# Optimization experiments

Hardware: AMD Instinct MI355X
Metric: run time of the kernel (lower is better)

The kernel has to match this reference:

```python
import jax, jax.numpy as jnp
import numpy as np

NEG_SLOPE = 0.2
K_L = 0.5
K_G = 0.5
TEMP_G = 1e-3


def _leaky(v):
    return jnp.where(v >= 0, v, NEG_SLOPE * v)


def _topk_row_mask(scores, keep):
    # scores: [n, n, h]; torch.topk(dim=0) -> indices [keep, n] per head,
    # then head_mask[indices, :] = 1 selects whole ROWS (any column hit).
    n = scores.shape[0]
    s = jnp.transpose(scores, (1, 2, 0))        # [n_cols, h, n_rows]
    _, idx = jax.lax.top_k(s, keep)             # [n_cols, h, keep]

    def per_head(idx_h):                        # idx_h: [n_cols, keep]
        return jnp.zeros((n,), scores.dtype).at[idx_h.reshape(-1)].set(1.0)

    rows = jax.vmap(per_head, in_axes=1, out_axes=0)(idx)  # [h, n_rows]
    return jnp.transpose(rows)[:, None, :]      # [n_rows, 1, h] broadcast over cols


def setup_inputs() -> dict:
    key = jax.random.key(0)
    ks = jax.random.split(key, 8)
    n, in_f, feat_dim = 1024, 256, 128
    H, F = 4, 64                                # n_heads, n_hidden (out_features=256)
    feats = jax.random.normal(ks[0], (n, feat_dim), dtype=jnp.float32)
    x = jax.random.normal(ks[1], (n, in_f), dtype=jnp.float32)
    adj = jax.random.randint(ks[2], (n, n, 1), 0, 2).astype(jnp.int32)
    sc = 0.05
    W_l = jax.random.normal(ks[3], (in_f, H * F), dtype=jnp.float32) * sc
    W_r = jax.random.normal(ks[4], (in_f, H * F), dtype=jnp.float32) * sc
    attn_w = jax.random.normal(ks[5], (F,), dtype=jnp.float32) * sc
    W_delta = jax.random.normal(ks[6], (2 * F, F), dtype=jnp.float32) * sc
    b_delta = jnp.zeros((F,), dtype=jnp.float32)
    return {"feats": feats, "x": x, "adj": adj, "W_l": W_l, "W_r": W_r,
            "attn_w": attn_w, "W_delta": W_delta, "b_delta": b_delta}


def reference(feats, x, adj, W_l, W_r, attn_w, W_delta, b_delta):
    n = x.shape[0]
    F = attn_w.shape[0]
    H = W_l.shape[1] // F
    g_l = (x @ W_l).reshape(n, H, F)
    g_r = (x @ W_r).reshape(n, H, F)
    # g_sum[i, j] = g_l[j] + g_r[i]  (repeat vs repeat_interleave ordering)
    g_sum = g_r[:, None, :, :] + g_l[None, :, :, :]          # [n, n, H, F]
    e = jnp.einsum('ijhf,f->ijh', _leaky(g_sum), attn_w)     # [n, n, H]

    mask_adj = adj > 0                                        # [n, n, 1]
    a_l = jax.nn.softmax(jnp.where(mask_adj, e, -jnp.inf), axis=1)
    a_1nd = a_l * mask_adj.astype(e.dtype)

    keep_l = int(n * (1.0 - K_L))
    a_filt = a_1nd * _topk_row_mask(a_1nd, keep_l)
    attn_local = jnp.einsum('ijh,jhf->ihf', a_filt, g_r)     # [n, H, F]

    omega = jax.nn.softmax(e, axis=1)
    fn = (feats - feats.min(axis=0)) / (feats.max(axis=0) - feats.min(axis=0))
    fn = jnp.where(jnp.isnan(fn), 0.0, fn)
    g_rn = (g_r - g_r.min(axis=0)) / (g_r.max(axis=0) - g_r.min(axis=0))
    nf = jnp.linalg.norm(fn, axis=1)                          # [n] (index j)
    ng = jnp.linalg.norm(g_rn, axis=2)                        # [n, H] (index i)
    alpha = jax.nn.softmax(jnp.abs(nf[None, :, None] - ng[:, None, :]), axis=1)
    gamma = 0.5 * (omega + (1.0 - alpha))

    keep_g = int(n * (1.0 - K_G))
    gf = gamma * _topk_row_mask(gamma, keep_g)
    gf = jax.nn.softmax(jnp.where(gf == 0, 1e-10, gf) / TEMP_G, axis=1)
    attn_global = jnp.einsum('ijh,jhf->ihf', gf, g_r)         # [n, H, F]

    inter = _leaky(jnp.concatenate([attn_local, attn_global], axis=2) @ W_delta + b_delta)
    delta = jax.nn.softmax(inter, axis=1)                     # softmax over heads (torch dim=1)
    attn_res = delta * attn_local + (1.0 - delta) * attn_global
    return attn_res.reshape(n, H * F)
```

## Files before the change

### kernel.cpp

```cpp
#include <hip/hip_runtime.h>
#include <cstdint>
#include <cstddef>

#define N 1024
#define HN 4
#define FDIM 64
#define KSEL 512
#define FLT_MAX_ 3.402823466e+38f

__device__ __forceinline__ float wred_sum(float v){
#pragma unroll
  for(int o=32;o>0;o>>=1) v += __shfl_down(v,o,64);
  return v;
}
__device__ __forceinline__ float bfly_sum(float v){
#pragma unroll
  for(int o=1;o<64;o<<=1) v += __shfl_xor(v,o,64);
  return v;
}
__device__ __forceinline__ float bfly_max(float v){
#pragma unroll
  for(int o=1;o<64;o<<=1) v = fmaxf(v,__shfl_xor(v,o,64));
  return v;
}
__device__ __forceinline__ int bfly_sumi(int v){
#pragma unroll
  for(int o=1;o<64;o<<=1) v += __shfl_xor(v,o,64);
  return v;
}
__device__ __forceinline__ float bred_sum(float v, float* scr){
  int t=threadIdx.x;
  v = wred_sum(v);
  __syncthreads();
  if((t&63)==0) scr[t>>6]=v;
  __syncthreads();
  return (scr[0]+scr[1])+(scr[2]+scr[3]);
}

__global__ __launch_bounds__(256) void stage1(const float* __restrict__ x,
                                              const float* __restrict__ W_l,
                                              const float* __restrict__ W_r,
                                              const int* __restrict__ adj,
                                              const float* __restrict__ feats,
                                              float* __restrict__ g_l,
                                              float* __restrict__ g_r,
                                              unsigned* __restrict__ adjbit,
                                              int* __restrict__ masks,
                                              float* __restrict__ pmin_f,
                                              float* __restrict__ pmax_f){
  int bx = blockIdx.x, t = threadIdx.x;
  if(bx < 512){
    const float* __restrict__ W = (bx >= 256) ? W_r : W_l;
    float* __restrict__ g = (bx >= 256) ? g_r : g_l;
    int i0 = (bx & 255)*4;
    float acc[4] = {0.f,0.f,0.f,0.f};
#pragma unroll 8
    for(int k=0;k<256;k++){
      float w = W[(size_t)k*256 + t];
#pragma unroll
      for(int r=0;r<4;r++) acc[r] = fmaf(x[(size_t)(i0+r)*256 + k], w, acc[r]);
    }
#pragma unroll
    for(int r=0;r<4;r++) g[(size_t)(i0+r)*256 + t] = acc[r];
  } else if(bx < 1536){
    int i = bx - 512, w = t>>6, lane = t&63;
    if(i < 32) masks[i*256 + t] = 0;
#pragma unroll
    for(int it=0; it<4; it++){
      int j = w*256 + it*64 + lane;
      int v = adj[(size_t)i*N + j];
      unsigned long long mb = __ballot(v > 0);
      if(lane == 0){
        adjbit[i*32 + w*8 + it*2]     = (unsigned)mb;
        adjbit[i*32 + w*8 + it*2 + 1] = (unsigned)(mb >> 32);
      }
    }
  } else {
    int chunk = bx - 1536;
    if(t < 128){
      float lo = FLT_MAX_, hi = -FLT_MAX_;
      int r0 = chunk*64;
      for(int r=0;r<64;r++){
        float v = feats[(size_t)(r0+r)*128 + t];
        lo = fminf(lo,v); hi = fmaxf(hi,v);
      }
      pmin_f[chunk*128+t]=lo; pmax_f[chunk*128+t]=hi;
    }
  }
}

__global__ __launch_bounds__(256) void stage2(const float* __restrict__ g_l,
                                              const float* __restrict__ g_r,
                                              const float* __restrict__ attn_w,
                                              const float* __restrict__ feats,
                                              const float* __restrict__ pmin_f, const float* __restrict__ pmax_f,
                                              float* __restrict__ pmin_g, float* __restrict__ pmax_g,
                                              float* __restrict__ nf,
                                              float* __restrict__ e,
                                              float* __restrict__ eT){
  __shared__ __align__(16) float smem[2*64*68 + 128];
  int bx = blockIdx.x, t = threadIdx.x;
  if(bx < 1024){
    float* grs = smem;
    float* gls = smem + 64*68;
    float* aw  = smem + 2*64*68;
    float* aw2 = aw + 64;
    int h = bx >> 8, i0 = ((bx>>4)&15)*64, j0 = (bx&15)*64;
    if(t < 64){ float w = attn_w[t]; aw[t]=w; aw2[t]=0.2f*w; }
#pragma unroll
    for(int k=0;k<16;k++){
      int idx = t + k*256; int r = idx>>6, f = idx&63;
      grs[r*68+f] = g_r[(size_t)(i0+r)*256 + h*64 + f];
      gls[r*68+f] = g_l[(size_t)(j0+r)*256 + h*64 + f];
    }
    __syncthreads();
    int tj = t&15, ti = t>>4;
    float acc[4][4];
#pragma unroll
    for(int a=0;a<4;a++)
#pragma unroll
      for(int b=0;b<4;b++) acc[a][b]=0.f;
    for(int fc=0; fc<64; fc+=4){
      float4 wv  = *(float4*)&aw[fc];
      float4 wv2 = *(float4*)&aw2[fc];
      float4 ga4[4], gb4[4];
#pragma unroll
      for(int a=0;a<4;a++) ga4[a] = *(float4*)&grs[(ti*4+a)*68+fc];
#pragma unroll
      for(int b=0;b<4;b++) gb4[b] = *(float4*)&gls[(tj+16*b)*68+fc];
#pragma unroll
      for(int a=0;a<4;a++)
#pragma unroll
        for(int b=0;b<4;b++){
          float s0 = ga4[a].x + gb4[b].x;
          float s1 = ga4[a].y + gb4[b].y;
          float s2 = ga4[a].z + gb4[b].z;
          float s3 = ga4[a].w + gb4[b].w;
          acc[a][b] = fmaf(s0, (s0>=0.f)?wv.x:wv2.x, acc[a][b]);
          acc[a][b] = fmaf(s1, (s1>=0.f)?wv.y:wv2.y, acc[a][b]);
          acc[a][b] = fmaf(s2, (s2>=0.f)?wv.z:wv2.z, acc[a][b]);
          acc[a][b] = fmaf(s3, (s3>=0.f)?wv.w:wv2.w, acc[a][b]);
        }
    }
#pragma unroll
    for(int a=0;a<4;a++)
#pragma unroll
      for(int b=0;b<4;b++){
        int i = i0 + ti*4 + a, j = j0 + tj + 16*b;
        e[((size_t)h*N + i)*N + j] = acc[a][b];
      }
    __syncthreads();
    float* esT = smem;
#pragma unroll
    for(int a=0;a<4;a++)
#pragma unroll
      for(int b=0;b<4;b++)
        esT[(tj + 16*b)*68 + ti*4 + a] = acc[a][b];
    __syncthreads();
#pragma unroll
    for(int k=0;k<4;k++){
      int jl = (t>>4) + 16*k, ilx = (t&15)*4;
      *(float4*)(eT + ((size_t)h*N + j0 + jl)*N + i0 + ilx) = *(float4*)&esT[jl*68 + ilx];
    }
  } else if(bx < 1040){
    int chunk = bx - 1024;
    float lo = FLT_MAX_, hi = -FLT_MAX_;
    int r0 = chunk*64;
    for(int r=0;r<64;r++){
      float v = g_r[(size_t)(r0+r)*256 + t];
      lo = fminf(lo,v); hi = fmaxf(hi,v);
    }
    pmin_g[chunk*256+t]=lo; pmax_g[chunk*256+t]=hi;
  } else {
    int i = bx - 1040;
    float* scr = smem;
    float u = 0.f;
    if(t < 128){
      float lo = FLT_MAX_, hi = -FLT_MAX_;
#pragma unroll
      for(int k=0;k<16;k++){
        lo = fminf(lo, pmin_f[k*128+t]);
        hi = fmaxf(hi, pmax_f[k*128+t]);
      }
      float d = hi - lo;
      float v = feats[(size_t)i*128 + t];
      u = (d==0.f) ? 0.f : (v - lo)/d;
    }
    float tot = bred_sum(u*u, scr);
    if(t==0) nf[i] = sqrtf(tot);
  }
}

__global__ __launch_bounds__(256) void row_stats(const float* __restrict__ e,
                                                 const unsigned* __restrict__ adjbit,
                                                 const float* __restrict__ nf,
                                                 const float* __restrict__ g_r,
                                                 const float* __restrict__ pmin_g, const float* __restrict__ pmax_g,
                                                 float* __restrict__ ng,
                                                 float* __restrict__ mlA, float* __restrict__ islA,
                                                 float* __restrict__ moA, float* __restrict__ isoA,
                                                 float* __restrict__ maA, float* __restrict__ isaA,
                                                 float* __restrict__ mgA, float* __restrict__ sgA){
  int i = blockIdx.x, t = threadIdx.x, h = t>>6, lane = t&63;
  float glo = FLT_MAX_, ghi = -FLT_MAX_;
#pragma unroll
  for(int k=0;k<16;k++){
    glo = fminf(glo, pmin_g[k*256 + h*64 + lane]);
    ghi = fmaxf(ghi, pmax_g[k*256 + h*64 + lane]);
  }
  float dg = ghi - glo;
  float ug = (g_r[(size_t)i*256 + h*64 + lane] - glo)/dg;
  float ngv = sqrtf(bfly_sum(ug*ug));
  if(lane==0) ng[h*N + i] = ngv;

  size_t base = ((size_t)h*N + i)*N;
  float er[16], nfr[16];
  unsigned nib[4];
#pragma unroll
  for(int c=0;c<4;c++){
    float4 e4 = *(const float4*)(e  + base + c*256 + lane*4);
    float4 n4 = *(const float4*)(nf + c*256 + lane*4);
    er[c*4+0]=e4.x; er[c*4+1]=e4.y; er[c*4+2]=e4.z; er[c*4+3]=e4.w;
    nfr[c*4+0]=n4.x; nfr[c*4+1]=n4.y; nfr[c*4+2]=n4.z; nfr[c*4+3]=n4.w;
    nib[c] = (adjbit[i*32 + c*8 + (lane>>3)] >> ((lane&7)*4)) & 0xFu;
  }
  float ml=-FLT_MAX_, mo=-FLT_MAX_, ma=-FLT_MAX_;
#pragma unroll
  for(int c=0;c<4;c++)
#pragma unroll
    for(int k=0;k<4;k++){
      int q = c*4+k;
      float ev = er[q];
      mo = fmaxf(mo, ev);
      if((nib[c]>>k)&1) ml = fmaxf(ml, ev);
      ma = fmaxf(ma, fabsf(nfr[q]-ngv));
    }
  ml = bfly_max(ml); mo = bfly_max(mo); ma = bfly_max(ma);
  float sl=0.f, so=0.f, sa=0.f;
#pragma unroll
  for(int c=0;c<4;c++)
#pragma unroll
    for(int k=0;k<4;k++){
      int q = c*4+k;
      float ev = er[q];
      so += __expf(ev-mo);
      if((nib[c]>>k)&1) sl += __expf(ev-ml);
      sa += __expf(fabsf(nfr[q]-ngv)-ma);
    }
  sl = bfly_sum(sl); so = bfly_sum(so); sa = bfly_sum(sa);
  float isl = 1.f/sl, iso = 1.f/so, isa = 1.f/sa;
  float gg[16];
  float mg = -FLT_MAX_;
#pragma unroll
  for(int q=0;q<16;q++){
    float ev = er[q];
    float omega = __expf(ev-mo)*iso;
    float alpha = __expf(fabsf(nfr[q]-ngv)-ma)*isa;
    float g = 0.5f*(omega + 1.f - alpha);
    gg[q] = g;
    mg = fmaxf(mg, g);
  }
  mg = bfly_max(mg);
  float sg = 0.f;
#pragma unroll
  for(int q=0;q<16;q++) sg += __expf((gg[q]-mg)/1e-3f);
  sg = bfly_sum(sg);
  if(lane==0){
    mlA[h*N+i]=ml; islA[h*N+i]=isl;
    moA[h*N+i]=mo; isoA[h*N+i]=iso;
    maA[h*N+i]=ma; isaA[h*N+i]=isa;
    mgA[h*N+i]=mg; sgA[h*N+i]=sg;
  }
}

__device__ __forceinline__ void select_top(const unsigned* ur, int* hw,
                                           int* __restrict__ mask, int base, int lane){
  int np = 0;
#pragma unroll
  for(int q=0;q<16;q++) np += (ur[q] != 0u) ? 1 : 0;
  int cnt_pos = bfly_sumi(np);

  unsigned T; int tneed; int tiecnt = -1;
  if(cnt_pos < KSEL){
    T = 0u; tneed = KSEL - cnt_pos;
  } else {
    unsigned prefix = 0; int kth = KSEL;
#pragma unroll
    for(int b=3;b>=0;b--){
      *(int4*)&hw[lane*4] = make_int4(0,0,0,0);
#pragma unroll
      for(int q=0;q<16;q++){
        unsigned u = ur[q];
        bool act = (b==3) || ((u >> (8*(b+1))) == prefix);
        if(act){
          int bucket = (u >> (8*b)) & 0xFF;
          unsigned long long mball = __ballot(true);
          int lead = __ffsll(mball) - 1;
          int maj = __shfl(bucket, lead, 64);
          if(bucket == maj){
            int cnt = (int)__popcll(__ballot(true));
            if(lane == lead) atomicAdd(&hw[maj], cnt);
          } else {
            atomicAdd(&hw[bucket], 1);
          }
        }
      }
      int4 hv = *(int4*)&hw[lane*4];
      int s = hv.x+hv.y+hv.z+hv.w;
      int P = s;
#pragma unroll
      for(int off=1; off<64; off<<=1){
        int q2 = __shfl_up(P, off, 64);
        if(lane >= off) P += q2;
      }
      int total = __shfl(P, 63, 64);
      int suffChunk  = total - (P - s);
      int suffChunkN = total - P;
      bool cross = (suffChunk >= kth) && (suffChunkN < kth);
      int selb=0, newk=0, tcnt=0;
      if(cross){
        int s3 = suffChunkN + hv.w;
        int s2 = s3 + hv.z;
        int s1 = s2 + hv.y;
        if(s3 >= kth){ selb=4*lane+3; newk = kth - suffChunkN; tcnt=hv.w; }
        else if(s2 >= kth){ selb=4*lane+2; newk = kth - s3; tcnt=hv.z; }
        else if(s1 >= kth){ selb=4*lane+1; newk = kth - s2; tcnt=hv.y; }
        else { selb=4*lane; newk = kth - s1; tcnt=hv.x; }
      }
      unsigned long long cm = __ballot(cross);
      int csrc = __ffsll(cm) - 1;
      selb   = __shfl(selb, csrc, 64);
      kth    = __shfl(newk, csrc, 64);
      tiecnt = __shfl(tcnt, csrc, 64);
      prefix = (prefix << 8) | (unsigned)selb;
    }
    T = prefix; tneed = kth;
  }

  if(tiecnt == tneed){
#pragma unroll
    for(int c=0;c<4;c++)
#pragma unroll
      for(int k2=0;k2<4;k2++){
        int i = c*256 + lane*4 + k2;
        if(ur[c*4+k2] >= T) mask[base + i] = 1;
      }
  } else {
    int run_base = 0;
#pragma unroll
    for(int c=0;c<4;c++){
      int tc=0;
#pragma unroll
      for(int k2=0;k2<4;k2++) tc += (ur[c*4+k2]==T)?1:0;
      int pc = tc;
#pragma unroll
      for(int off=1; off<64; off<<=1){
        int q2 = __shfl_up(pc, off, 64);
        if(lane >= off) pc += q2;
      }
      int ctot = __shfl(pc, 63, 64);
      int run = run_base + pc - tc;
#pragma unroll
      for(int k2=0;k2<4;k2++){
        int i = c*256 + lane*4 + k2;
        unsigned u = ur[c*4+k2];
        bool sel = (u > T) || (u == T && run < tneed);
        run += (u==T)?1:0;
        if(sel) mask[base + i] = 1;
      }
      run_base += ctot;
    }
  }
}

__global__ __launch_bounds__(256) void colselect7(const float* __restrict__ eT,
                                                  const unsigned* __restrict__ adjbit,
                                                  const float* __restrict__ nf,
                                                  const float* __restrict__ mlA, const float* __restrict__ islA,
                                                  const float* __restrict__ moA, const float* __restrict__ isoA,
                                                  const float* __restrict__ maA, const float* __restrict__ isaA,
                                                  const float* __restrict__ ngA,
                                                  int* __restrict__ mask_l,
                                                  int* __restrict__ mask_g){
  __shared__ __align__(16) int hist[4][256];
  int t = threadIdx.x, w = t>>6, lane = t&63;
  int col = blockIdx.x*4 + w;
  int h = col >> 10, jc = col & 1023;
  const float* __restrict__ src = eT + (size_t)col * (size_t)N;

  float ev[16];
  unsigned abits = 0;
  int wo = jc >> 5; unsigned bm = 1u << (jc & 31);
#pragma unroll
  for(int c=0;c<4;c++){
    float4 e4 = ((const float4*)src)[c*64 + lane];
    ev[c*4+0]=e4.x; ev[c*4+1]=e4.y; ev[c*4+2]=e4.z; ev[c*4+3]=e4.w;
#pragma unroll
    for(int k=0;k<4;k++){
      int i = c*256 + lane*4 + k;
      abits |= (adjbit[i*32 + wo] & bm) ? (1u << (c*4+k)) : 0u;
    }
  }
  unsigned ur[16];
#pragma unroll
  for(int c=0;c<4;c++){
    int ib = (h<<10) + c*256 + lane*4;
    float4 ml4 = *(const float4*)(mlA+ib);
    float4 il4 = *(const float4*)(islA+ib);
    float mlv[4] = {ml4.x,ml4.y,ml4.z,ml4.w};
    float ilv[4] = {il4.x,il4.y,il4.z,il4.w};
#pragma unroll
    for(int k=0;k<4;k++){
      float a = ((abits>>(c*4+k))&1u) ? __expf(ev[c*4+k]-mlv[k])*ilv[k] : 0.f;
      ur[c*4+k] = __float_as_uint(a);
    }
  }
  select_top(ur, hist[w], mask_l, h<<10, lane);
  float nfv = nf[jc];
#pragma unroll
  for(int c=0;c<4;c++){
    int ib = (h<<10) + c*256 + lane*4;
    float4 mo4 = *(const float4*)(moA+ib);
    float4 io4 = *(const float4*)(isoA+ib);
    float4 ma4 = *(const float4*)(maA+ib);
    float4 ia4 = *(const float4*)(isaA+ib);
    float4 ng4 = *(const float4*)(ngA+ib);
    float mov[4]={mo4.x,mo4.y,mo4.z,mo4.w}, iov[4]={io4.x,io4.y,io4.z,io4.w};
    float mav[4]={ma4.x,ma4.y,ma4.z,ma4.w}, iav[4]={ia4.x,ia4.y,ia4.z,ia4.w};
    float ngv[4]={ng4.x,ng4.y,ng4.z,ng4.w};
#pragma unroll
    for(int k=0;k<4;k++){
      float omega = __expf(ev[c*4+k]-mov[k])*iov[k];
      float alpha = __expf(fabsf(nfv-ngv[k])-mav[k])*iav[k];
      float g = 0.5f*(omega + 1.f - alpha);
      ur[c*4+k] = __float_as_uint(g);
    }
  }
  select_top(ur, hist[w], mask_g, h<<10, lane);
}

__global__ __launch_bounds__(256) void attn_mm2(const float* __restrict__ eT,
                                                const float* __restrict__ g_r,
                                                const unsigned* __restrict__ adjbit,
                                                const float* __restrict__ nf,
                                                const float* __restrict__ mlA, const float* __restrict__ islA,
                                                const float* __restrict__ moA, const float* __restrict__ isoA,
                                                const float* __restrict__ maA, const float* __restrict__ isaA,
                                                const float* __restrict__ ngA,
                                                const float* __restrict__ mgA, const float* __restrict__ sgA,
                                                const int* __restrict__ mask_g,
                                                float* __restrict__ partL,
                                                float* __restrict__ partG){
  __shared__ __align__(16) float a_t[2][32][36];
  __shared__ __align__(16) float p_t[2][32][36];
  __shared__ __align__(16) float b_s[2][32][68];
  int i0 = blockIdx.x*32, h = blockIdx.y, s = blockIdx.z, j0 = s*128;
  int t = threadIdx.x;
  int il = t & 31, jq = t >> 5;
  int gi = h*N + i0 + il;
  float ml_r = mlA[gi], il_r = islA[gi];
  float mo_r = moA[gi], io_r = isoA[gi];
  float ma_r = maA[gi], ia_r = isaA[gi];
  float ng_r = ngA[gi];
  float mg_r = mgA[gi], isg_r = 1.f/sgA[gi];
  int   mgf_r = mask_g[gi];
  int fq = t & 15, iq = t >> 4;
  int jb2a = t>>4, d4a = t&15;
  int idxb = t + 256, jb2b = idxb>>4, d4b = idxb&15;

  float e0,e1,e2,e3; unsigned aw; float4 nf4, vb0, vb1;
  {
    int jb = j0;
    size_t ebase = ((size_t)h*N + jb + jq*4)*(size_t)N + i0 + il;
    e0 = eT[ebase]; e1 = eT[ebase+N]; e2 = eT[ebase+2*N]; e3 = eT[ebase+3*N];
    aw = adjbit[(size_t)(i0+il)*32 + s*4 + 0];
    nf4 = *(const float4*)(nf + jb + jq*4);
    vb0 = *(const float4*)(g_r + (size_t)(jb+jb2a)*256 + h*64 + d4a*4);
    vb1 = *(const float4*)(g_r + (size_t)(jb+jb2b)*256 + h*64 + d4b*4);
  }
  {
    const float inv = 1.f/1024.f;
    float evs[4] = {e0,e1,e2,e3};
    float nfsv[4] = {nf4.x,nf4.y,nf4.z,nf4.w};
#pragma unroll
    for(int c=0;c<4;c++){
      int jl = jq*4 + c;
      float a = ((aw >> jl) & 1u) ? __expf(evs[c]-ml_r)*il_r : 0.f;
      float omega = __expf(evs[c]-mo_r)*io_r;
      float alpha = __expf(fabsf(nfsv[c]-ng_r)-ma_r)*ia_r;
      float g = 0.5f*(omega + 1.f - alpha);
      float p = mgf_r ? __expf((g-mg_r)/1e-3f)*isg_r : inv;
      a_t[0][jl][il] = a;
      p_t[0][jl][il] = p;
    }
    *(float4*)&b_s[0][jb2a][d4a*4] = vb0;
    *(float4*)&b_s[0][jb2b][d4b*4] = vb1;
  }
  float4 accL[2], accG[2];
#pragma unroll
  for(int r=0;r<2;r++){ accL[r]=make_float4(0,0,0,0); accG[r]=make_float4(0,0,0,0); }

  for(int sub=0; sub<4; sub++){
    int cur = sub & 1;
    __syncthreads();
    if(sub < 3){
      int jb = j0 + (sub+1)*32;
      size_t ebase = ((size_t)h*N + jb + jq*4)*(size_t)N + i0 + il;
      e0 = eT[ebase]; e1 = eT[ebase+N]; e2 = eT[ebase+2*N]; e3 = eT[ebase+3*N];
      aw = adjbit[(size_t)(i0+il)*32 + s*4 + sub + 1];
      nf4 = *(const float4*)(nf + jb + jq*4);
      vb0 = *(const float4*)(g_r + (size_t)(jb+jb2a)*256 + h*64 + d4a*4);
      vb1 = *(const float4*)(g_r + (size_t)(jb+jb2b)*256 + h*64 + d4b*4);
    }
#pragma unroll 8
    for(int j=0;j<32;j++){
      float4 bv = *(float4*)&b_s[cur][j][fq*4];
      float2 av = *(float2*)&a_t[cur][j][iq*2];
      float2 pv = *(float2*)&p_t[cur][j][iq*2];
      accL[0].x = fmaf(av.x, bv.x, accL[0].x); accL[0].y = fmaf(av.x, bv.y, accL[0].y);
      accL[0].z = fmaf(av.x, bv.z, accL[0].z); accL[0].w = fmaf(av.x, bv.w, accL[0].w);
      accL[1].x = fmaf(av.y, bv.x, accL[1].x); accL[1].y = fmaf(av.y, bv.y, accL[1].y);
      accL[1].z = fmaf(av.y, bv.z, accL[1].z); accL[1].w = fmaf(av.y, bv.w, accL[1].w);
      accG[0].x = fmaf(pv.x, bv.x, accG[0].x); accG[0].y = fmaf(pv.x, bv.y, accG[0].y);
      accG[0].z = fmaf(pv.x, bv.z, accG[0].z); accG[0].w = fmaf(pv.x, bv.w, accG[0].w);
      accG[1].x = fmaf(pv.y, bv.x, accG[1].x); accG[1].y = fmaf(pv.y, bv.y, accG[1].y);
      accG[1].z = fmaf(pv.y, bv.z, accG[1].z); accG[1].w = fmaf(pv.y, bv.w, accG[1].w);
    }
    if(sub < 3){
      int nxt = 1 - cur;
      const float inv = 1.f/1024.f;
      float evs[4] = {e0,e1,e2,e3};
      float nfsv[4] = {nf4.x,nf4.y,nf4.z,nf4.w};
#pragma unroll
      for(int c=0;c<4;c++){
        int jl = jq*4 + c;
        float a = ((aw >> jl) & 1u) ? __expf(evs[c]-ml_r)*il_r : 0.f;
        float omega = __expf(evs[c]-mo_r)*io_r;
        float alpha = __expf(fabsf(nfsv[c]-ng_r)-ma_r)*ia_r;
        float g = 0.5f*(omega + 1.f - alpha);
        float p = mgf_r ? __expf((g-mg_r)/1e-3f)*isg_r : inv;
        a_t[nxt][jl][il] = a;
        p_t[nxt][jl][il] = p;
      }
      *(float4*)&b_s[nxt][jb2a][d4a*4] = vb0;
      *(float4*)&b_s[nxt][jb2b][d4b*4] = vb1;
    }
  }
#pragma unroll
  for(int r=0;r<2;r++){
    int i = i0 + iq*2 + r;
    size_t o = ((size_t)s*N + i)*256 + h*64 + fq*4;
    *(float4*)&partL[o] = accL[r];
    *(float4*)&partG[o] = accG[r];
  }
}

__global__ __launch_bounds__(256) void epilogue(const float* __restrict__ partL,
                                                const float* __restrict__ partG,
                                                const int* __restrict__ mask_l,
                                                const float* __restrict__ W_delta,
                                                const float* __restrict__ b_delta,
                                                float* __restrict__ out){
  __shared__ float cat[4][128];
  __shared__ float inter_s[4][64];
  int i = blockIdx.x, t = threadIdx.x;
  int h = t>>6, f = t&63;
  float sl = 0.f, sg = 0.f;
#pragma unroll
  for(int s2=0;s2<8;s2++){
    size_t o = ((size_t)s2*N + i)*256 + h*64 + f;
    sl += partL[o];
    sg += partG[o];
  }
  if(!mask_l[h*N + i]) sl = 0.f;
  cat[h][f]      = sl;
  cat[h][64 + f] = sg;
  __syncthreads();
  float d = b_delta[f];
  for(int c=0;c<128;c++) d = fmaf(cat[h][c], W_delta[(size_t)c*64 + f], d);
  d = (d >= 0.f) ? d : 0.2f*d;
  inter_s[h][f] = d;
  __syncthreads();
  float m = inter_s[0][f];
#pragma unroll
  for(int hh=1;hh<4;hh++) m = fmaxf(m, inter_s[hh][f]);
  float ssum = 0.f;
#pragma unroll
  for(int hh=0;hh<4;hh++) ssum += __expf(inter_s[hh][f]-m);
  float delta = __expf(d - m)/ssum;
  out[(size_t)i*256 + h*64 + f] = delta*sl + (1.f - delta)*sg;
}

extern "C" void kernel_launch(void* const* d_in, const int* in_sizes, int n_in,
                              void* d_out, int out_size, void* d_ws, size_t ws_size,
                              hipStream_t stream) {
  const float* feats  = (const float*)d_in[0];
  const float* x      = (const float*)d_in[1];
  const int*   adj    = (const int*)  d_in[2];
  const float* W_l    = (const float*)d_in[3];
  const float* W_r    = (const float*)d_in[4];
  const float* attn_w = (const float*)d_in[5];
  const float* W_delta= (const float*)d_in[6];
  const float* b_delta= (const float*)d_in[7];
  float* out = (float*)d_out;

  float* ws = (float*)d_ws;
  size_t off = 0;
  float* g_l   = ws+off; off += (size_t)N*256;
  float* g_r   = ws+off; off += (size_t)N*256;
  float* e     = ws+off; off += (size_t)HN*N*N;
  float* eT    = ws+off; off += (size_t)HN*N*N;
  float* partL = ws+off; off += (size_t)8*N*256;
  float* partG = ws+off; off += (size_t)8*N*256;
  float* pmin_f= ws+off; off += 16*128;
  float* pmax_f= ws+off; off += 16*128;
  float* pmin_g= ws+off; off += 16*256;
  float* pmax_g= ws+off; off += 16*256;
  float* nf    = ws+off; off += N;
  float* ng    = ws+off; off += (size_t)HN*N;
  float* mlA   = ws+off; off += (size_t)HN*N;
  float* islA  = ws+off; off += (size_t)HN*N;
  float* moA   = ws+off; off += (size_t)HN*N;
  float* isoA  = ws+off; off += (size_t)HN*N;
  float* maA   = ws+off; off += (size_t)HN*N;
  float* isaA  = ws+off; off += (size_t)HN*N;
  float* mgA   = ws+off; off += (size_t)HN*N;
  float* sgA   = ws+off; off += (size_t)HN*N;
  int* mask_l  = (int*)(ws+off); off += (size_t)HN*N;
  int* mask_g  = (int*)(ws+off); off += (size_t)HN*N;
  unsigned* adjbit = (unsigned*)(ws+off); off += (size_t)N*32;

  stage1<<<1552, 256, 0, stream>>>(x, W_l, W_r, adj, feats, g_l, g_r, adjbit, mask_l, pmin_f, pmax_f);

  stage2<<<2064, 256, 0, stream>>>(g_l, g_r, attn_w, feats, pmin_f, pmax_f,
                                   pmin_g, pmax_g, nf, e, eT);

  row_stats<<<N, 256, 0, stream>>>(e, adjbit, nf, g_r, pmin_g, pmax_g, ng,
                                   mlA, islA, moA, isoA, maA, isaA, mgA, sgA);

  colselect7<<<1024, 256, 0, stream>>>(eT, adjbit, nf, mlA, islA, moA, isoA,
                                       maA, isaA, ng, mask_l, mask_g);

  attn_mm2<<<dim3(32,HN,8), 256, 0, stream>>>(eT, g_r, adjbit, nf,
                                              mlA, islA, moA, isoA, maA, isaA, ng,
                                              mgA, sgA, mask_g, partL, partG);

  epilogue<<<N, 256, 0, stream>>>(partL, partG, mask_l, W_delta, b_delta, out);
}
```

Measured before the change: 199.9 us.

## Split column top-k select across local/global and use bitwise radix threshold search

New measurement: 199.1 us. About the same (-0.4%).

```diff
diff --git a/kernel.cpp b/kernel.cpp
--- a/kernel.cpp
+++ b/kernel.cpp
@@ -273,71 +273,9 @@
   }
 }
 
-__device__ __forceinline__ void select_top(const unsigned* ur, int* hw,
+__device__ __forceinline__ void apply_mask(const unsigned* ur, unsigned T, int tneed, int EQ,
                                            int* __restrict__ mask, int base, int lane){
-  int np = 0;
-#pragma unroll
-  for(int q=0;q<16;q++) np += (ur[q] != 0u) ? 1 : 0;
-  int cnt_pos = bfly_sumi(np);
-
-  unsigned T; int tneed; int tiecnt = -1;
-  if(cnt_pos < KSEL){
-    T = 0u; tneed = KSEL - cnt_pos;
-  } else {
-    unsigned prefix = 0; int kth = KSEL;
-#pragma unroll
-    for(int b=3;b>=0;b--){
-      *(int4*)&hw[lane*4] = make_int4(0,0,0,0);
-#pragma unroll
-      for(int q=0;q<16;q++){
-        unsigned u = ur[q];
-        bool act = (b==3) || ((u >> (8*(b+1))) == prefix);
-        if(act){
-          int bucket = (u >> (8*b)) & 0xFF;
-          unsigned long long mball = __ballot(true);
-          int lead = __ffsll(mball) - 1;
-          int maj = __shfl(bucket, lead, 64);
-          if(bucket == maj){
-            int cnt = (int)__popcll(__ballot(true));
-            if(lane == lead) atomicAdd(&hw[maj], cnt);
-          } else {
-            atomicAdd(&hw[bucket], 1);
-          }
-        }
-      }
-      int4 hv = *(int4*)&hw[lane*4];
-      int s = hv.x+hv.y+hv.z+hv.w;
-      int P = s;
-#pragma unroll
-      for(int off=1; off<64; off<<=1){
-        int q2 = __shfl_up(P, off, 64);
-        if(lane >= off) P += q2;
-      }
-      int total = __shfl(P, 63, 64);
-      int suffChunk  = total - (P - s);
-      int suffChunkN = total - P;
-      bool cross = (suffChunk >= kth) && (suffChunkN < kth);
-      int selb=0, newk=0, tcnt=0;
-      if(cross){
-        int s3 = suffChunkN + hv.w;
-        int s2 = s3 + hv.z;
-        int s1 = s2 + hv.y;
-        if(s3 >= kth){ selb=4*lane+3; newk = kth - suffChunkN; tcnt=hv.w; }
-        else if(s2 >= kth){ selb=4*lane+2; newk = kth - s3; tcnt=hv.z; }
-        else if(s1 >= kth){ selb=4*lane+1; newk = kth - s2; tcnt=hv.y; }
-        else { selb=4*lane; newk = kth - s1; tcnt=hv.x; }
-      }
-      unsigned long long cm = __ballot(cross);
-      int csrc = __ffsll(cm) - 1;
-      selb   = __shfl(selb, csrc, 64);
-      kth    = __shfl(newk, csrc, 64);
-      tiecnt = __shfl(tcnt, csrc, 64);
-      prefix = (prefix << 8) | (unsigned)selb;
-    }
-    T = prefix; tneed = kth;
-  }
-
-  if(tiecnt == tneed){
+  if(EQ == tneed){
 #pragma unroll
     for(int c=0;c<4;c++)
 #pragma unroll
@@ -373,7 +311,7 @@
   }
 }
 
-__global__ __launch_bounds__(256) void colselect7(const float* __restrict__ eT,
+__global__ __launch_bounds__(256) void colselect8(const float* __restrict__ eT,
                                                   const unsigned* __restrict__ adjbit,
                                                   const float* __restrict__ nf,
                                                   const float* __restrict__ mlA, const float* __restrict__ islA,
@@ -382,61 +320,78 @@
                                                   const float* __restrict__ ngA,
                                                   int* __restrict__ mask_l,
                                                   int* __restrict__ mask_g){
-  __shared__ __align__(16) int hist[4][256];
   int t = threadIdx.x, w = t>>6, lane = t&63;
-  int col = blockIdx.x*4 + w;
-  int h = col >> 10, jc = col & 1023;
-  const float* __restrict__ src = eT + (size_t)col * (size_t)N;
+  int gcol = blockIdx.x*4 + w;
+  int z  = gcol >> 12;
+  int hj = gcol & 4095;
+  int h  = hj >> 10, jc = hj & 1023;
+  const float* __restrict__ src = eT + (size_t)hj * (size_t)N;
 
   float ev[16];
-  unsigned abits = 0;
-  int wo = jc >> 5; unsigned bm = 1u << (jc & 31);
 #pragma unroll
   for(int c=0;c<4;c++){
     float4 e4 = ((const float4*)src)[c*64 + lane];
     ev[c*4+0]=e4.x; ev[c*4+1]=e4.y; ev[c*4+2]=e4.z; ev[c*4+3]=e4.w;
-#pragma unroll
-    for(int k=0;k<4;k++){
-      int i = c*256 + lane*4 + k;
-      abits |= (adjbit[i*32 + wo] & bm) ? (1u << (c*4+k)) : 0u;
-    }
   }
   unsigned ur[16];
-#pragma unroll
-  for(int c=0;c<4;c++){
-    int ib = (h<<10) + c*256 + lane*4;
-    float4 ml4 = *(const float4*)(mlA+ib);
-    float4 il4 = *(const float4*)(islA+ib);
-    float mlv[4] = {ml4.x,ml4.y,ml4.z,ml4.w};
-    float ilv[4] = {il4.x,il4.y,il4.z,il4.w};
-#pragma unroll
-    for(int k=0;k<4;k++){
-      float a = ((abits>>(c*4+k))&1u) ? __expf(ev[c*4+k]-mlv[k])*ilv[k] : 0.f;
-      ur[c*4+k] = __float_as_uint(a);
-    }
-  }
-  select_top(ur, hist[w], mask_l, h<<10, lane);
-  float nfv = nf[jc];
-#pragma unroll
-  for(int c=0;c<4;c++){
-    int ib = (h<<10) + c*256 + lane*4;
-    float4 mo4 = *(const float4*)(moA+ib);
-    float4 io4 = *(const float4*)(isoA+ib);
-    float4 ma4 = *(const float4*)(maA+ib);
-    float4 ia4 = *(const float4*)(isaA+ib);
-    float4 ng4 = *(const float4*)(ngA+ib);
-    float mov[4]={mo4.x,mo4.y,mo4.z,mo4.w}, iov[4]={io4.x,io4.y,io4.z,io4.w};
-    float mav[4]={ma4.x,ma4.y,ma4.z,ma4.w}, iav[4]={ia4.x,ia4.y,ia4.z,ia4.w};
-    float ngv[4]={ng4.x,ng4.y,ng4.z,ng4.w};
-#pragma unroll
-    for(int k=0;k<4;k++){
-      float omega = __expf(ev[c*4+k]-mov[k])*iov[k];
-      float alpha = __expf(fabsf(nfv-ngv[k])-mav[k])*iav[k];
-      float g = 0.5f*(omega + 1.f - alpha);
-      ur[c*4+k] = __float_as_uint(g);
-    }
-  }
-  select_top(ur, hist[w], mask_g, h<<10, lane);
+  if(z == 0){
+    int wo = jc >> 5; unsigned bm = 1u << (jc & 31);
+#pragma unroll
+    for(int c=0;c<4;c++){
+      int ib = (h<<10) + c*256 + lane*4;
+      float4 ml4 = *(const float4*)(mlA+ib);
+      float4 il4 = *(const float4*)(islA+ib);
+      float mlv[4] = {ml4.x,ml4.y,ml4.z,ml4.w};
+      float ilv[4] = {il4.x,il4.y,il4.z,il4.w};
+#pragma unroll
+      for(int k=0;k<4;k++){
+        int i = c*256 + lane*4 + k;
+        float a = (adjbit[i*32 + wo] & bm) ? __expf(ev[c*4+k]-mlv[k])*ilv[k] : 0.f;
+        ur[c*4+k] = __float_as_uint(a);
+      }
+    }
+  } else {
+    float nfv = nf[jc];
+#pragma unroll
+    for(int c=0;c<4;c++){
+      int ib = (h<<10) + c*256 + lane*4;
+      float4 mo4 = *(const float4*)(moA+ib);
+      float4 io4 = *(const float4*)(isoA+ib);
+      float4 ma4 = *(const float4*)(maA+ib);
+      float4 ia4 = *(const float4*)(isaA+ib);
+      float4 ng4 = *(const float4*)(ngA+ib);
+      float mov[4]={mo4.x,mo4.y,mo4.z,mo4.w}, iov[4]={io4.x,io4.y,io4.z,io4.w};
+      float mav[4]={ma4.x,ma4.y,ma4.z,ma4.w}, iav[4]={ia4.x,ia4.y,ia4.z,ia4.w};
+      float ngv[4]={ng4.x,ng4.y,ng4.z,ng4.w};
+#pragma unroll
+      for(int k=0;k<4;k++){
+        float omega = __expf(ev[c*4+k]-mov[k])*iov[k];
+        float alpha = __expf(fabsf(nfv-ngv[k])-mav[k])*iav[k];
+        float g = 0.5f*(omega + 1.f - alpha);
+        ur[c*4+k] = __float_as_uint(g);
+      }
+    }
+  }
+
+  unsigned prefix = 0u;
+  for(int b=30; b>=0; b--){
+    unsigned cand = prefix | (1u<<b);
+    int c = 0;
+#pragma unroll
+    for(int q=0;q<16;q++) c += (ur[q] >= cand) ? 1 : 0;
+    c = bfly_sumi(c);
+    if(c >= KSEL) prefix = cand;
+  }
+  unsigned T = prefix;
+  int pk = 0;
+#pragma unroll
+  for(int q=0;q<16;q++) pk += (ur[q] > T) ? 2048 : ((ur[q]==T) ? 1 : 0);
+  pk = bfly_sumi(pk);
+  int GT = pk >> 11, EQ = pk & 2047;
+  int tneed = KSEL - GT;
+
+  int* __restrict__ mask = z ? mask_g : mask_l;
+  apply_mask(ur, T, tneed, EQ, mask, h<<10, lane);
 }
 
 __global__ __launch_bounds__(256) void attn_mm2(const float* __restrict__ eT,
@@ -638,7 +593,7 @@
   row_stats<<<N, 256, 0, stream>>>(e, adjbit, nf, g_r, pmin_g, pmax_g, ng,
                                    mlA, islA, moA, isoA, maA, isaA, mgA, sgA);
 
-  colselect7<<<1024, 256, 0, stream>>>(eT, adjbit, nf, mlA, islA, moA, isoA,
+  colselect8<<<2048, 256, 0, stream>>>(eT, adjbit, nf, mlA, islA, moA, isoA,
                                        maA, isaA, ng, mask_l, mask_g);
 
   attn_mm2<<<dim3(32,HN,8), 256, 0, stream>>>(eT, g_r, adjbit, nf,
```
